# Kernel optimization log

Hardware: AMD Instinct MI355X
Metric: run time of the kernel (lower is better)

The kernel has to match this reference:

```python
import math
import jax, jax.numpy as jnp
import numpy as np

EMBED_DIM = 1024
N_HEADS = 16
HEAD_DIM = EMBED_DIM // N_HEADS
B, T = 4, 2048


def setup_inputs() -> dict:
    key = jax.random.key(0)
    k1, k2, k3 = jax.random.split(key, 3)
    scale_in = 1.0 / math.sqrt(EMBED_DIM)
    return {
        "x": jax.random.normal(k1, (B, T, EMBED_DIM), dtype=jnp.float32),
        "direction": 0,  # 0=FORWARD (causal), 1=RETRODICTION (anti-causal), 2=CORRECTION (causal)
        "qkv_w": jax.random.normal(k2, (EMBED_DIM, 3 * EMBED_DIM), dtype=jnp.float32) * scale_in,
        "qkv_b": jnp.zeros((3 * EMBED_DIM,), dtype=jnp.float32),
        "proj_w": jax.random.normal(k3, (EMBED_DIM, EMBED_DIM), dtype=jnp.float32) * scale_in,
        "proj_b": jnp.zeros((EMBED_DIM,), dtype=jnp.float32),
    }


def reference(x, direction, qkv_w, qkv_b, proj_w, proj_b):
    Bx, Tx, C = x.shape
    qkv = x @ qkv_w + qkv_b                        # [B,T,3C]
    q, k, v = jnp.split(qkv, 3, axis=-1)
    # [B,T,C] -> [B,H,T,D]
    def heads(t):
        return t.reshape(Bx, Tx, N_HEADS, HEAD_DIM).transpose(0, 2, 1, 3)
    q, k, v = heads(q), heads(k), heads(v)
    scale = 1.0 / math.sqrt(HEAD_DIM)
    attn = jnp.einsum('bhqd,bhkd->bhqk', q, k) * scale
    rows = jnp.arange(Tx)[:, None]
    cols = jnp.arange(Tx)[None, :]
    if direction == 1:  # RETRODICTION -> anti-causal (upper triangular allowed)
        mask = cols >= rows
    else:               # FORWARD / CORRECTION -> causal
        mask = cols <= rows
    attn = jnp.where(mask[None, None], attn, -jnp.inf)
    attn = jax.nn.softmax(attn, axis=-1)  # dropout p=0 -> identity
    out = jnp.einsum('bhqk,bhkd->bhqd', attn, v)   # [B,H,T,D]
    out = out.transpose(0, 2, 1, 3).reshape(Bx, Tx, C)
    return out @ proj_w + proj_b
```

## Files before the change

kernel.cpp:

```cpp
#include <hip/hip_runtime.h>
#include <math.h>

typedef __bf16 bf16_t;
typedef bf16_t bf16x8 __attribute__((ext_vector_type(8)));
typedef bf16_t bf16x4 __attribute__((ext_vector_type(4)));
typedef float  f32x4  __attribute__((ext_vector_type(4)));
typedef float  floatv4 __attribute__((ext_vector_type(4)));

#define AS1 __attribute__((address_space(1)))
#define AS3 __attribute__((address_space(3)))

static __device__ __forceinline__ void gld_lds16(const void* g, void* l) {
  __builtin_amdgcn_global_load_lds((const AS1 unsigned int*)g,
                                   (AS3 unsigned int*)l, 16, 0, 0);
}
static __device__ __forceinline__ void block_sync() {
  asm volatile("" ::: "memory");
  __builtin_amdgcn_s_barrier();
  asm volatile("" ::: "memory");
}

__global__ __launch_bounds__(256) void k_cast(const float* __restrict__ in,
                                              bf16_t* __restrict__ out, int n4) {
  int i = blockIdx.x * 256 + threadIdx.x;
  if (i >= n4) return;
  floatv4 v = ((const floatv4*)in)[i];
  bf16x4 o;
  o.x = (bf16_t)v.x; o.y = (bf16_t)v.y; o.z = (bf16_t)v.z; o.w = (bf16_t)v.w;
  ((bf16x4*)out)[i] = o;
}

__global__ __launch_bounds__(256) void k_transpose_cast(const float* __restrict__ in,
                                                        bf16_t* __restrict__ out,
                                                        int R, int Cc) {
  __shared__ float tile[32][33];
  int c0 = blockIdx.x * 32, r0 = blockIdx.y * 32;
  int tx = threadIdx.x, ty = threadIdx.y;
#pragma unroll
  for (int i = 0; i < 32; i += 8)
    tile[ty + i][tx] = in[(size_t)(r0 + ty + i) * Cc + c0 + tx];
  __syncthreads();
#pragma unroll
  for (int i = 0; i < 32; i += 8)
    out[(size_t)(c0 + ty + i) * R + r0 + tx] = (bf16_t)tile[tx][ty + i];
}

__global__ __launch_bounds__(256) void k_gemm_qkv(
    const bf16_t* __restrict__ A, const bf16_t* __restrict__ Bt,
    const float* __restrict__ bias,
    bf16_t* __restrict__ qo, bf16_t* __restrict__ ko, bf16_t* __restrict__ vto) {
  const int K = 1024;
  __shared__ __align__(16) char smem[33792];
  const int m0 = blockIdx.x * 128, n0 = blockIdx.y * 128;
  const int t = threadIdx.x, lane = t & 63, w = t >> 6;
  const int wr = w >> 1, wc = w & 1;
  const int ln15 = lane & 15, lhi = lane >> 4;

  f32x4 acc[4][4];
#pragma unroll
  for (int m = 0; m < 4; ++m)
#pragma unroll
    for (int n = 0; n < 4; ++n) acc[m][n] = (f32x4){0.f, 0.f, 0.f, 0.f};

  const bf16_t* aSrc = A + (size_t)(m0 + w * 16 + ln15) * K + lhi * 8;
  const bf16_t* bSrc = Bt + (size_t)(n0 + w * 16 + ln15) * K + lhi * 8;
  char* dstA = smem + t * 16;

  auto stageG = [&](int k0, int buf) {
    char* base = dstA + buf * 16384;
    gld_lds16(aSrc + k0, base);
    gld_lds16(aSrc + 64 * K + k0, base + 4096);
    gld_lds16(bSrc + k0, base + 8192);
    gld_lds16(bSrc + 64 * K + k0, base + 12288);
  };

  stageG(0, 0);
  asm volatile("s_waitcnt vmcnt(0)" ::: "memory");
  block_sync();
  int buf = 0;
#pragma unroll 2
  for (int it = 0; it < 32; ++it) {
    if (it + 1 < 32) stageG((it + 1) * 32, buf ^ 1);
    const bf16_t* Asb = (const bf16_t*)(smem + buf * 16384);
    const bf16_t* Bsb = (const bf16_t*)(smem + buf * 16384 + 8192);
    bf16x8 af[4], bfr[4];
#pragma unroll
    for (int m = 0; m < 4; ++m)
      af[m] = *(const bf16x8*)(Asb + (wr * 4 + m) * 512 + lane * 8);
#pragma unroll
    for (int n = 0; n < 4; ++n)
      bfr[n] = *(const bf16x8*)(Bsb + (wc * 4 + n) * 512 + lane * 8);
#pragma unroll
    for (int m = 0; m < 4; ++m)
#pragma unroll
      for (int n = 0; n < 4; ++n)
        acc[m][n] = __builtin_amdgcn_mfma_f32_16x16x32_bf16(af[m], bfr[n], acc[m][n], 0, 0, 0);
    asm volatile("s_waitcnt vmcnt(0)" ::: "memory");
    block_sync();
    buf ^= 1;
  }

  bf16_t* L = (bf16_t*)smem;
  const int which = n0 >> 10;
  const float bscale = (which == 0) ? 0.18033688011112042f : 1.0f;
#pragma unroll
  for (int n = 0; n < 4; ++n) {
    const int col = wc * 64 + n * 16 + ln15;
    const float bv = bias[n0 + col];
#pragma unroll
    for (int m = 0; m < 4; ++m)
#pragma unroll
      for (int j = 0; j < 4; ++j) {
        const int row = wr * 64 + m * 16 + lhi * 4 + j;
        const bf16_t ob = (bf16_t)((acc[m][n][j] + bv) * bscale);
        if (which == 2) L[col * 132 + row] = ob;
        else            L[row * 132 + col] = ob;
      }
  }
  block_sync();
  const int bq = m0 >> 11, ttb = m0 & 2047;
  if (which == 2) {
#pragma unroll
    for (int c = 0; c < 8; ++c) {
      const int idx = c * 256 + t;
      const int vcol = idx >> 4, r8 = (idx & 15) * 8;
      bf16x8 v8 = *(const bf16x8*)&L[vcol * 132 + r8];
      const int cc = (n0 + vcol) & 1023;
      const int hh = cc >> 6, d = cc & 63;
      *(bf16x8*)&vto[((size_t)(bq * 16 + hh) * 64 + d) * 2048 + ttb + r8] = v8;
    }
  } else {
    bf16_t* dst = (which == 0) ? qo : ko;
#pragma unroll
    for (int c = 0; c < 8; ++c) {
      const int idx = c * 256 + t;
      const int row = idx >> 4, c8 = (idx & 15) * 8;
      bf16x8 v8 = *(const bf16x8*)&L[row * 132 + c8];
      const int cc = (n0 & 1023) + c8;
      const int hh = cc >> 6, d = cc & 63;
      *(bf16x8*)&dst[((size_t)(bq * 16 + hh) * 2048 + ttb + row) * 64 + d] = v8;
    }
  }
}

__global__ __launch_bounds__(256) void k_attn3(
    const bf16_t* __restrict__ q, const bf16_t* __restrict__ k,
    const bf16_t* __restrict__ vt, const int* __restrict__ dirp,
    bf16_t* __restrict__ a2) {
  const int T = 2048;
  __shared__ __align__(16) bf16_t smem[16384];
  const int bh = blockIdx.x, b = bh >> 4, h = bh & 15;
  const int jb = blockIdx.y;
  const int t = threadIdx.x, lane = t & 63, w = t >> 6;
  const int ln15 = lane & 15, lhi = lane >> 4;
  const bool anti = (*dirp == 1);

  const bf16_t* kbase = k + (size_t)bh * T * 64;
  const bf16_t* vbase = vt + (size_t)bh * 64 * T;

  auto stage = [&](int kc0, int buf) {
    char* Kd = (char*)smem + buf * 16384;
    char* Vd = Kd + 8192;
#pragma unroll
    for (int s = 0; s < 2; ++s) {
      const int qk = s * 4 + (t >> 6);
      const int krow = kc0 + (qk >> 2) * 32 + ((qk >> 1) & 1) * 4 +
                       ((lane & 15) >> 2) * 8 + (lane & 3);
      const int kcolb = (lane >> 4) * 16 + (qk & 1) * 64;
      gld_lds16((const char*)kbase + (size_t)krow * 128 + kcolb,
                Kd + s * 4096 + t * 16);
      const int gv = qk;
      const int vd = (gv & 3) * 16 + (lane & 15);
      gld_lds16((const char*)vbase + (size_t)vd * 4096 + (size_t)kc0 * 2 +
                    (gv >> 2) * 64 + (lane >> 4) * 16,
                Vd + s * 4096 + t * 16);
    }
  };

#pragma unroll 1
  for (int sel = 0; sel < 2; ++sel) {
    const int qt = sel ? (31 - jb) : jb;
    const int q0 = qt * 64 + w * 16;
    const int qrow = q0 + ln15;

    const bf16_t* qp = q + ((size_t)bh * T + qrow) * 64 + lhi * 8;
    bf16x8 qf0 = *(const bf16x8*)qp;
    bf16x8 qf1 = *(const bf16x8*)(qp + 32);

    f32x4 acc[4];
#pragma unroll
    for (int g = 0; g < 4; ++g) acc[g] = (f32x4){0.f, 0.f, 0.f, 0.f};
    float mrun = -3.0e38f, lrun = 0.f;

    const int kt0 = anti ? qt : 0;
    const int nb = anti ? (32 - qt) : (qt + 1);

    stage(kt0 * 64, 0);
#pragma unroll 1
    for (int i = 0; i < nb; ++i) {
      const int kt = kt0 + i;
      const int buf = i & 1;
      if (i + 1 < nb) {
        stage((kt + 1) * 64, buf ^ 1);
        asm volatile("s_waitcnt vmcnt(4)" ::: "memory");
      } else {
        asm volatile("s_waitcnt vmcnt(0)" ::: "memory");
      }
      block_sync();
      const bf16_t* Kb = smem + buf * 8192;
      const bf16_t* Vb = Kb + 4096;

      float sc[16];
#pragma unroll
      for (int kh = 0; kh < 2; ++kh) {
        bf16x8 k0 = *(const bf16x8*)(Kb + (kh * 4 + 0) * 512 + lane * 8);
        bf16x8 k1 = *(const bf16x8*)(Kb + (kh * 4 + 1) * 512 + lane * 8);
        bf16x8 k2 = *(const bf16x8*)(Kb + (kh * 4 + 2) * 512 + lane * 8);
        bf16x8 k3 = *(const bf16x8*)(Kb + (kh * 4 + 3) * 512 + lane * 8);
        const f32x4 zz = (f32x4){0.f, 0.f, 0.f, 0.f};
        f32x4 slo = __builtin_amdgcn_mfma_f32_16x16x32_bf16(k0, qf0, zz, 0, 0, 0);
        slo = __builtin_amdgcn_mfma_f32_16x16x32_bf16(k1, qf1, slo, 0, 0, 0);
        f32x4 shi = __builtin_amdgcn_mfma_f32_16x16x32_bf16(k2, qf0, zz, 0, 0, 0);
        shi = __builtin_amdgcn_mfma_f32_16x16x32_bf16(k3, qf1, shi, 0, 0, 0);
#pragma unroll
        for (int j = 0; j < 4; ++j) {
          sc[kh * 8 + j] = slo[j];
          sc[kh * 8 + 4 + j] = shi[j];
        }
      }
      if (kt == qt) {
#pragma unroll
        for (int e = 0; e < 16; ++e) {
          const int col = kt * 64 + (e >> 3) * 32 + lhi * 8 + (e & 7);
          const bool ok = anti ? (col >= qrow) : (col <= qrow);
          sc[e] = ok ? sc[e] : -3.0e38f;
        }
      }
      float lmax = sc[0];
#pragma unroll
      for (int e = 1; e < 16; ++e) lmax = fmaxf(lmax, sc[e]);
      if (!__all(lmax <= mrun + 8.f)) {
        float vm = lmax;
        vm = fmaxf(vm, __shfl_xor(vm, 16));
        vm = fmaxf(vm, __shfl_xor(vm, 32));
        const float mn = fmaxf(mrun, vm);
        const float al = __builtin_amdgcn_exp2f(mrun - mn);
        lrun *= al;
#pragma unroll
        for (int g = 0; g < 4; ++g) acc[g] *= al;
        mrun = mn;
      }
      bf16x8 pb0, pb1;
      float rs = 0.f;
#pragma unroll
      for (int e = 0; e < 8; ++e) {
        float p = __builtin_amdgcn_exp2f(sc[e] - mrun);
        rs += p; pb0[e] = (bf16_t)p;
      }
#pragma unroll
      for (int e = 0; e < 8; ++e) {
        float p = __builtin_amdgcn_exp2f(sc[8 + e] - mrun);
        rs += p; pb1[e] = (bf16_t)p;
      }
      lrun += rs;
#pragma unroll
      for (int dg = 0; dg < 4; ++dg) {
        bf16x8 v0 = *(const bf16x8*)(Vb + dg * 512 + lane * 8);
        acc[dg] = __builtin_amdgcn_mfma_f32_16x16x32_bf16(v0, pb0, acc[dg], 0, 0, 0);
      }
#pragma unroll
      for (int dg = 0; dg < 4; ++dg) {
        bf16x8 v1 = *(const bf16x8*)(Vb + (4 + dg) * 512 + lane * 8);
        acc[dg] = __builtin_amdgcn_mfma_f32_16x16x32_bf16(v1, pb1, acc[dg], 0, 0, 0);
      }
      block_sync();
    }

    lrun += __shfl_xor(lrun, 16);
    lrun += __shfl_xor(lrun, 32);
    const float inv = __builtin_amdgcn_rcpf(lrun);
    bf16_t* op = a2 + ((size_t)b * T + qrow) * 1024 + h * 64 + lhi * 4;
#pragma unroll
    for (int g = 0; g < 4; ++g) {
      bf16x4 o4;
#pragma unroll
      for (int jx = 0; jx < 4; ++jx) o4[jx] = (bf16_t)(acc[g][jx] * inv);
      *(bf16x4*)(op + g * 16) = o4;
    }
  }
}

__global__ __launch_bounds__(256) void k_gemm_proj(
    const bf16_t* __restrict__ A, const bf16_t* __restrict__ Bt,
    const float* __restrict__ bias, float* __restrict__ out) {
  const int K = 1024;
  __shared__ __align__(16) char smem[32768];
  const int m0 = blockIdx.x * 128, n0 = blockIdx.y * 128;
  const int t = threadIdx.x, lane = t & 63, w = t >> 6;
  const int wr = w >> 1, wc = w & 1;
  const int ln15 = lane & 15, lhi = lane >> 4;

  f32x4 acc[4][4];
#pragma unroll
  for (int m = 0; m < 4; ++m)
#pragma unroll
    for (int n = 0; n < 4; ++n) acc[m][n] = (f32x4){0.f, 0.f, 0.f, 0.f};

  const bf16_t* aSrc = A + (size_t)(m0 + w * 16 + ln15) * K + lhi * 8;
  const bf16_t* bSrc = Bt + (size_t)(n0 + w * 16 + ln15) * K + lhi * 8;
  char* dstA = smem + t * 16;

  auto stageG = [&](int k0, int buf) {
    char* base = dstA + buf * 16384;
    gld_lds16(aSrc + k0, base);
    gld_lds16(aSrc + 64 * K + k0, base + 4096);
    gld_lds16(bSrc + k0, base + 8192);
    gld_lds16(bSrc + 64 * K + k0, base + 12288);
  };

  stageG(0, 0);
  asm volatile("s_waitcnt vmcnt(0)" ::: "memory");
  block_sync();
  int buf = 0;
#pragma unroll 2
  for (int it = 0; it < 32; ++it) {
    if (it + 1 < 32) stageG((it + 1) * 32, buf ^ 1);
    const bf16_t* Asb = (const bf16_t*)(smem + buf * 16384);
    const bf16_t* Bsb = (const bf16_t*)(smem + buf * 16384 + 8192);
    bf16x8 af[4], bfr[4];
#pragma unroll
    for (int m = 0; m < 4; ++m)
      af[m] = *(const bf16x8*)(Asb + (wr * 4 + m) * 512 + lane * 8);
#pragma unroll
    for (int n = 0; n < 4; ++n)
      bfr[n] = *(const bf16x8*)(Bsb + (wc * 4 + n) * 512 + lane * 8);
#pragma unroll
    for (int m = 0; m < 4; ++m)
#pragma unroll
      for (int n = 0; n < 4; ++n)
        acc[m][n] = __builtin_amdgcn_mfma_f32_16x16x32_bf16(af[m], bfr[n], acc[m][n], 0, 0, 0);
    asm volatile("s_waitcnt vmcnt(0)" ::: "memory");
    block_sync();
    buf ^= 1;
  }
#pragma unroll
  for (int n = 0; n < 4; ++n) {
    const int col = n0 + wc * 64 + n * 16 + ln15;
    const float bv = bias[col];
#pragma unroll
    for (int m = 0; m < 4; ++m)
#pragma unroll
      for (int j = 0; j < 4; ++j) {
        const int row = m0 + wr * 64 + m * 16 + lhi * 4 + j;
        out[(size_t)row * 1024 + col] = acc[m][n][j] + bv;
      }
  }
}

extern "C" void kernel_launch(void* const* d_in, const int* in_sizes, int n_in,
                              void* d_out, int out_size, void* d_ws, size_t ws_size,
                              hipStream_t stream) {
  (void)in_sizes; (void)n_in; (void)out_size; (void)ws_size;
  const float* x      = (const float*)d_in[0];
  const int*   dirp   = (const int*)d_in[1];
  const float* qkv_w  = (const float*)d_in[2];
  const float* qkv_b  = (const float*)d_in[3];
  const float* proj_w = (const float*)d_in[4];
  const float* proj_b = (const float*)d_in[5];
  float* out = (float*)d_out;

  char* ws = (char*)d_ws;
  bf16_t* xb   = (bf16_t*)(ws);
  bf16_t* wq_t = (bf16_t*)(ws + 16777216);
  bf16_t* wp_t = (bf16_t*)(ws + 23068672);
  bf16_t* qb   = (bf16_t*)(ws + 25165824);
  bf16_t* kb   = (bf16_t*)(ws + 41943040);
  bf16_t* vtb  = (bf16_t*)(ws + 58720256);
  bf16_t* a2   = xb;

  k_cast<<<8192, 256, 0, stream>>>(x, xb, 2097152);
  k_transpose_cast<<<dim3(96, 32), dim3(32, 8), 0, stream>>>(qkv_w, wq_t, 1024, 3072);
  k_transpose_cast<<<dim3(32, 32), dim3(32, 8), 0, stream>>>(proj_w, wp_t, 1024, 1024);
  k_gemm_qkv<<<dim3(64, 24), 256, 0, stream>>>(xb, wq_t, qkv_b, qb, kb, vtb);
  k_attn3<<<dim3(64, 16), 256, 0, stream>>>(qb, kb, vtb, dirp, a2);
  k_gemm_proj<<<dim3(64, 8), 256, 0, stream>>>(a2, wp_t, proj_b, out);
}
```

Measured before the change: 223.5 us.

## Enlarge GEMM tiles to 256x128 with 512 threads and triple-buffered BK=64 pipeline

Both the QKV and output-projection GEMMs move from 128x128 tiles with 256 threads, BK=32 and double buffering to 256x128 tiles with 512 threads (8 waves), BK=64 and a three-stage global-to-LDS pipeline. Partial vmcnt waits let two stages of loads stay in flight while one is computed, and s_setprio raises wave priority around the MFMA bursts. The aim is more reuse per LDS load, fewer barriers per unit of K, and better hiding of global latency. The cost is about 144KB of LDS per block, which allows only one block per CU. The projection grid shrinks to 256 blocks, which lowers occupancy and may leave load imbalance.

```diff
diff --git a/kernel.cpp b/kernel.cpp
--- a/kernel.cpp
+++ b/kernel.cpp
@@ -45,16 +45,17 @@
     out[(size_t)(c0 + ty + i) * R + r0 + tx] = (bf16_t)tile[tx][ty + i];
 }
 
-__global__ __launch_bounds__(256) void k_gemm_qkv(
+
+__global__ __launch_bounds__(512, 2) void k_gemm_qkv(
     const bf16_t* __restrict__ A, const bf16_t* __restrict__ Bt,
     const float* __restrict__ bias,
     bf16_t* __restrict__ qo, bf16_t* __restrict__ ko, bf16_t* __restrict__ vto) {
   const int K = 1024;
-  __shared__ __align__(16) char smem[33792];
-  const int m0 = blockIdx.x * 128, n0 = blockIdx.y * 128;
-  const int t = threadIdx.x, lane = t & 63, w = t >> 6;
-  const int wr = w >> 1, wc = w & 1;
+  __shared__ __align__(16) char smem[147456];
+  const int m0 = blockIdx.x * 256, n0 = blockIdx.y * 128;
+  const int t = threadIdx.x, lane = t & 63, wv = t >> 6;
   const int ln15 = lane & 15, lhi = lane >> 4;
+  const int wr = wv >> 1, wc = wv & 1;
 
   f32x4 acc[4][4];
 #pragma unroll
@@ -62,47 +63,64 @@
 #pragma unroll
     for (int n = 0; n < 4; ++n) acc[m][n] = (f32x4){0.f, 0.f, 0.f, 0.f};
 
-  const bf16_t* aSrc = A + (size_t)(m0 + w * 16 + ln15) * K + lhi * 8;
-  const bf16_t* bSrc = Bt + (size_t)(n0 + w * 16 + ln15) * K + lhi * 8;
-  char* dstA = smem + t * 16;
-
-  auto stageG = [&](int k0, int buf) {
-    char* base = dstA + buf * 16384;
-    gld_lds16(aSrc + k0, base);
-    gld_lds16(aSrc + 64 * K + k0, base + 4096);
-    gld_lds16(bSrc + k0, base + 8192);
-    gld_lds16(bSrc + 64 * K + k0, base + 12288);
+  const bf16_t* aSrc = A + (size_t)(m0 + (t >> 7) * 16 + ln15) * K + ((t >> 6) & 1) * 32 + lhi * 8;
+  const bf16_t* bSrc = Bt + (size_t)(n0 + (t >> 7) * 16 + ln15) * K + ((t >> 6) & 1) * 32 + lhi * 8;
+  const int dstOff = t * 16;
+
+  auto stage = [&](int k0, char* base) {
+#pragma unroll
+    for (int c = 0; c < 4; ++c)
+      gld_lds16(aSrc + (size_t)c * 64 * K + k0, base + c * 8192 + dstOff);
+#pragma unroll
+    for (int c = 0; c < 2; ++c)
+      gld_lds16(bSrc + (size_t)c * 64 * K + k0, base + 32768 + c * 8192 + dstOff);
   };
-
-  stageG(0, 0);
-  asm volatile("s_waitcnt vmcnt(0)" ::: "memory");
-  block_sync();
-  int buf = 0;
-#pragma unroll 2
-  for (int it = 0; it < 32; ++it) {
-    if (it + 1 < 32) stageG((it + 1) * 32, buf ^ 1);
-    const bf16_t* Asb = (const bf16_t*)(smem + buf * 16384);
-    const bf16_t* Bsb = (const bf16_t*)(smem + buf * 16384 + 8192);
-    bf16x8 af[4], bfr[4];
-#pragma unroll
-    for (int m = 0; m < 4; ++m)
-      af[m] = *(const bf16x8*)(Asb + (wr * 4 + m) * 512 + lane * 8);
-#pragma unroll
-    for (int n = 0; n < 4; ++n)
-      bfr[n] = *(const bf16x8*)(Bsb + (wc * 4 + n) * 512 + lane * 8);
-#pragma unroll
-    for (int m = 0; m < 4; ++m)
+  auto compute = [&](const char* base) {
+    const bf16_t* Ab = (const bf16_t*)base;
+    const bf16_t* Bb = (const bf16_t*)(base + 32768);
+#pragma unroll
+    for (int kk = 0; kk < 2; ++kk) {
+      bf16x8 af[4], bf[4];
+#pragma unroll
+      for (int m = 0; m < 4; ++m)
+        af[m] = *(const bf16x8*)(Ab + ((wr * 4 + m) * 2 + kk) * 512 + lane * 8);
 #pragma unroll
       for (int n = 0; n < 4; ++n)
-        acc[m][n] = __builtin_amdgcn_mfma_f32_16x16x32_bf16(af[m], bfr[n], acc[m][n], 0, 0, 0);
-    asm volatile("s_waitcnt vmcnt(0)" ::: "memory");
+        bf[n] = *(const bf16x8*)(Bb + ((wc * 4 + n) * 2 + kk) * 512 + lane * 8);
+      __builtin_amdgcn_s_setprio(1);
+#pragma unroll
+      for (int m = 0; m < 4; ++m)
+#pragma unroll
+        for (int n = 0; n < 4; ++n)
+          acc[m][n] = __builtin_amdgcn_mfma_f32_16x16x32_bf16(af[m], bf[n], acc[m][n], 0, 0, 0);
+      __builtin_amdgcn_s_setprio(0);
+    }
+  };
+
+  char* pc = smem;
+  char* p1 = smem + 49152;
+  char* p2 = smem + 98304;
+  stage(0, pc);
+  stage(64, p1);
+#pragma unroll 1
+  for (int it = 0; it < 16; ++it) {
+    if (it + 2 < 16) {
+      stage((it + 2) * 64, p2);
+      asm volatile("s_waitcnt vmcnt(12)" ::: "memory");
+    } else if (it + 1 < 16) {
+      asm volatile("s_waitcnt vmcnt(6)" ::: "memory");
+    } else {
+      asm volatile("s_waitcnt vmcnt(0)" ::: "memory");
+    }
     block_sync();
-    buf ^= 1;
-  }
-
-  bf16_t* L = (bf16_t*)smem;
+    compute(pc);
+    block_sync();
+    char* old = pc; pc = p1; p1 = p2; p2 = old;
+  }
+
   const int which = n0 >> 10;
   const float bscale = (which == 0) ? 0.18033688011112042f : 1.0f;
+  bf16_t* L = (bf16_t*)smem;
 #pragma unroll
   for (int n = 0; n < 4; ++n) {
     const int col = wc * 64 + n * 16 + ln15;
@@ -113,7 +131,7 @@
       for (int j = 0; j < 4; ++j) {
         const int row = wr * 64 + m * 16 + lhi * 4 + j;
         const bf16_t ob = (bf16_t)((acc[m][n][j] + bv) * bscale);
-        if (which == 2) L[col * 132 + row] = ob;
+        if (which == 2) L[col * 264 + row] = ob;
         else            L[row * 132 + col] = ob;
       }
   }
@@ -122,9 +140,9 @@
   if (which == 2) {
 #pragma unroll
     for (int c = 0; c < 8; ++c) {
-      const int idx = c * 256 + t;
-      const int vcol = idx >> 4, r8 = (idx & 15) * 8;
-      bf16x8 v8 = *(const bf16x8*)&L[vcol * 132 + r8];
+      const int idx = c * 512 + t;
+      const int vcol = idx >> 5, r8 = (idx & 31) * 8;
+      bf16x8 v8 = *(const bf16x8*)&L[vcol * 264 + r8];
       const int cc = (n0 + vcol) & 1023;
       const int hh = cc >> 6, d = cc & 63;
       *(bf16x8*)&vto[((size_t)(bq * 16 + hh) * 64 + d) * 2048 + ttb + r8] = v8;
@@ -133,7 +151,7 @@
     bf16_t* dst = (which == 0) ? qo : ko;
 #pragma unroll
     for (int c = 0; c < 8; ++c) {
-      const int idx = c * 256 + t;
+      const int idx = c * 512 + t;
       const int row = idx >> 4, c8 = (idx & 15) * 8;
       bf16x8 v8 = *(const bf16x8*)&L[row * 132 + c8];
       const int cc = (n0 & 1023) + c8;
@@ -290,15 +308,15 @@
   }
 }
 
-__global__ __launch_bounds__(256) void k_gemm_proj(
+__global__ __launch_bounds__(512, 2) void k_gemm_proj(
     const bf16_t* __restrict__ A, const bf16_t* __restrict__ Bt,
     const float* __restrict__ bias, float* __restrict__ out) {
   const int K = 1024;
-  __shared__ __align__(16) char smem[32768];
-  const int m0 = blockIdx.x * 128, n0 = blockIdx.y * 128;
-  const int t = threadIdx.x, lane = t & 63, w = t >> 6;
-  const int wr = w >> 1, wc = w & 1;
+  __shared__ __align__(16) char smem[147456];
+  const int m0 = blockIdx.x * 256, n0 = blockIdx.y * 128;
+  const int t = threadIdx.x, lane = t & 63, wv = t >> 6;
   const int ln15 = lane & 15, lhi = lane >> 4;
+  const int wr = wv >> 1, wc = wv & 1;
 
   f32x4 acc[4][4];
 #pragma unroll
@@ -306,43 +324,61 @@
 #pragma unroll
     for (int n = 0; n < 4; ++n) acc[m][n] = (f32x4){0.f, 0.f, 0.f, 0.f};
 
-  const bf16_t* aSrc = A + (size_t)(m0 + w * 16 + ln15) * K + lhi * 8;
-  const bf16_t* bSrc = Bt + (size_t)(n0 + w * 16 + ln15) * K + lhi * 8;
-  char* dstA = smem + t * 16;
-
-  auto stageG = [&](int k0, int buf) {
-    char* base = dstA + buf * 16384;
-    gld_lds16(aSrc + k0, base);
-    gld_lds16(aSrc + 64 * K + k0, base + 4096);
-    gld_lds16(bSrc + k0, base + 8192);
-    gld_lds16(bSrc + 64 * K + k0, base + 12288);
+  const bf16_t* aSrc = A + (size_t)(m0 + (t >> 7) * 16 + ln15) * K + ((t >> 6) & 1) * 32 + lhi * 8;
+  const bf16_t* bSrc = Bt + (size_t)(n0 + (t >> 7) * 16 + ln15) * K + ((t >> 6) & 1) * 32 + lhi * 8;
+  const int dstOff = t * 16;
+
+  auto stage = [&](int k0, char* base) {
+#pragma unroll
+    for (int c = 0; c < 4; ++c)
+      gld_lds16(aSrc + (size_t)c * 64 * K + k0, base + c * 8192 + dstOff);
+#pragma unroll
+    for (int c = 0; c < 2; ++c)
+      gld_lds16(bSrc + (size_t)c * 64 * K + k0, base + 32768 + c * 8192 + dstOff);
   };
-
-  stageG(0, 0);
-  asm volatile("s_waitcnt vmcnt(0)" ::: "memory");
-  block_sync();
-  int buf = 0;
-#pragma unroll 2
-  for (int it = 0; it < 32; ++it) {
-    if (it + 1 < 32) stageG((it + 1) * 32, buf ^ 1);
-    const bf16_t* Asb = (const bf16_t*)(smem + buf * 16384);
-    const bf16_t* Bsb = (const bf16_t*)(smem + buf * 16384 + 8192);
-    bf16x8 af[4], bfr[4];
-#pragma unroll
-    for (int m = 0; m < 4; ++m)
-      af[m] = *(const bf16x8*)(Asb + (wr * 4 + m) * 512 + lane * 8);
-#pragma unroll
-    for (int n = 0; n < 4; ++n)
-      bfr[n] = *(const bf16x8*)(Bsb + (wc * 4 + n) * 512 + lane * 8);
-#pragma unroll
-    for (int m = 0; m < 4; ++m)
+  auto compute = [&](const char* base) {
+    const bf16_t* Ab = (const bf16_t*)base;
+    const bf16_t* Bb = (const bf16_t*)(base + 32768);
+#pragma unroll
+    for (int kk = 0; kk < 2; ++kk) {
+      bf16x8 af[4], bf[4];
+#pragma unroll
+      for (int m = 0; m < 4; ++m)
+        af[m] = *(const bf16x8*)(Ab + ((wr * 4 + m) * 2 + kk) * 512 + lane * 8);
 #pragma unroll
       for (int n = 0; n < 4; ++n)
-        acc[m][n] = __builtin_amdgcn_mfma_f32_16x16x32_bf16(af[m], bfr[n], acc[m][n], 0, 0, 0);
-    asm volatile("s_waitcnt vmcnt(0)" ::: "memory");
+        bf[n] = *(const bf16x8*)(Bb + ((wc * 4 + n) * 2 + kk) * 512 + lane * 8);
+      __builtin_amdgcn_s_setprio(1);
+#pragma unroll
+      for (int m = 0; m < 4; ++m)
+#pragma unroll
+        for (int n = 0; n < 4; ++n)
+          acc[m][n] = __builtin_amdgcn_mfma_f32_16x16x32_bf16(af[m], bf[n], acc[m][n], 0, 0, 0);
+      __builtin_amdgcn_s_setprio(0);
+    }
+  };
+
+  char* pc = smem;
+  char* p1 = smem + 49152;
+  char* p2 = smem + 98304;
+  stage(0, pc);
+  stage(64, p1);
+#pragma unroll 1
+  for (int it = 0; it < 16; ++it) {
+    if (it + 2 < 16) {
+      stage((it + 2) * 64, p2);
+      asm volatile("s_waitcnt vmcnt(12)" ::: "memory");
+    } else if (it + 1 < 16) {
+      asm volatile("s_waitcnt vmcnt(6)" ::: "memory");
+    } else {
+      asm volatile("s_waitcnt vmcnt(0)" ::: "memory");
+    }
     block_sync();
-    buf ^= 1;
-  }
+    compute(pc);
+    block_sync();
+    char* old = pc; pc = p1; p1 = p2; p2 = old;
+  }
+
 #pragma unroll
   for (int n = 0; n < 4; ++n) {
     const int col = n0 + wc * 64 + n * 16 + ln15;
@@ -381,7 +417,7 @@
   k_cast<<<8192, 256, 0, stream>>>(x, xb, 2097152);
   k_transpose_cast<<<dim3(96, 32), dim3(32, 8), 0, stream>>>(qkv_w, wq_t, 1024, 3072);
   k_transpose_cast<<<dim3(32, 32), dim3(32, 8), 0, stream>>>(proj_w, wp_t, 1024, 1024);
-  k_gemm_qkv<<<dim3(64, 24), 256, 0, stream>>>(xb, wq_t, qkv_b, qb, kb, vtb);
+  k_gemm_qkv<<<dim3(32, 24), 512, 0, stream>>>(xb, wq_t, qkv_b, qb, kb, vtb);
   k_attn3<<<dim3(64, 16), 256, 0, stream>>>(qb, kb, vtb, dirp, a2);
-  k_gemm_proj<<<dim3(64, 8), 256, 0, stream>>>(a2, wp_t, proj_b, out);
-}
+  k_gemm_proj<<<dim3(32, 8), 512, 0, stream>>>(a2, wp_t, proj_b, out);
+}
```

Result: faster. 204.5 us (-8.5%).

## Widen QKV GEMM tile to 128x256 and add MFMA priority scheduling

Applied to the files above, without the earlier changes.

The QKV projection GEMM now computes a 128x256 output tile per block, with each wave owning a 128x64 strip so the A fragments are shared across a wider N. This halves the grid and raises reuse of each A load. Both GEMMs also wait on LDS explicitly, raise wave priority around the MFMA bursts, and set launch_bounds occupancy to 3. The epilogue is now split into two passes through LDS. Risks are higher register pressure from 32 accumulators per wave, fewer blocks in flight, and extra barriers in the epilogue.

```diff
diff --git a/kernel.cpp b/kernel.cpp
--- a/kernel.cpp
+++ b/kernel.cpp
@@ -45,101 +45,116 @@
     out[(size_t)(c0 + ty + i) * R + r0 + tx] = (bf16_t)tile[tx][ty + i];
 }
 
-__global__ __launch_bounds__(256) void k_gemm_qkv(
+
+__global__ __launch_bounds__(256, 3) void k_gemm_qkv(
     const bf16_t* __restrict__ A, const bf16_t* __restrict__ Bt,
     const float* __restrict__ bias,
     bf16_t* __restrict__ qo, bf16_t* __restrict__ ko, bf16_t* __restrict__ vto) {
   const int K = 1024;
-  __shared__ __align__(16) char smem[33792];
-  const int m0 = blockIdx.x * 128, n0 = blockIdx.y * 128;
-  const int t = threadIdx.x, lane = t & 63, w = t >> 6;
-  const int wr = w >> 1, wc = w & 1;
+  __shared__ __align__(16) char smem[49152];
+  const int m0 = blockIdx.x * 128, n0 = blockIdx.y * 256;
+  const int t = threadIdx.x, lane = t & 63, wv = t >> 6;
   const int ln15 = lane & 15, lhi = lane >> 4;
 
-  f32x4 acc[4][4];
-#pragma unroll
-  for (int m = 0; m < 4; ++m)
+  f32x4 acc[8][4];
+#pragma unroll
+  for (int m = 0; m < 8; ++m)
 #pragma unroll
     for (int n = 0; n < 4; ++n) acc[m][n] = (f32x4){0.f, 0.f, 0.f, 0.f};
 
-  const bf16_t* aSrc = A + (size_t)(m0 + w * 16 + ln15) * K + lhi * 8;
-  const bf16_t* bSrc = Bt + (size_t)(n0 + w * 16 + ln15) * K + lhi * 8;
-  char* dstA = smem + t * 16;
-
-  auto stageG = [&](int k0, int buf) {
-    char* base = dstA + buf * 16384;
-    gld_lds16(aSrc + k0, base);
-    gld_lds16(aSrc + 64 * K + k0, base + 4096);
-    gld_lds16(bSrc + k0, base + 8192);
-    gld_lds16(bSrc + 64 * K + k0, base + 12288);
+  const bf16_t* aS = A + (size_t)(m0 + wv * 16 + ln15) * K + lhi * 8;
+  const bf16_t* bS = Bt + (size_t)(n0 + wv * 16 + ln15) * K + lhi * 8;
+
+  auto stage = [&](int k0, char* buf) {
+    gld_lds16(aS + k0, buf + t * 16);
+    gld_lds16(aS + (size_t)64 * K + k0, buf + 4096 + t * 16);
+#pragma unroll
+    for (int r = 0; r < 4; ++r)
+      gld_lds16(bS + (size_t)r * 64 * K + k0, buf + 8192 + r * 4096 + t * 16);
   };
 
-  stageG(0, 0);
+  stage(0, smem);
   asm volatile("s_waitcnt vmcnt(0)" ::: "memory");
   block_sync();
-  int buf = 0;
-#pragma unroll 2
+
+#pragma unroll 1
   for (int it = 0; it < 32; ++it) {
-    if (it + 1 < 32) stageG((it + 1) * 32, buf ^ 1);
-    const bf16_t* Asb = (const bf16_t*)(smem + buf * 16384);
-    const bf16_t* Bsb = (const bf16_t*)(smem + buf * 16384 + 8192);
+    char* bufC = smem + (it & 1) * 24576;
+    char* bufN = smem + ((it + 1) & 1) * 24576;
+    if (it + 1 < 32) stage((it + 1) * 32, bufN);
+    const bf16_t* Ab = (const bf16_t*)bufC;
+    const bf16_t* Bb = (const bf16_t*)(bufC + 8192);
     bf16x8 af[4], bfr[4];
 #pragma unroll
-    for (int m = 0; m < 4; ++m)
-      af[m] = *(const bf16x8*)(Asb + (wr * 4 + m) * 512 + lane * 8);
-#pragma unroll
     for (int n = 0; n < 4; ++n)
-      bfr[n] = *(const bf16x8*)(Bsb + (wc * 4 + n) * 512 + lane * 8);
-#pragma unroll
-    for (int m = 0; m < 4; ++m)
-#pragma unroll
-      for (int n = 0; n < 4; ++n)
-        acc[m][n] = __builtin_amdgcn_mfma_f32_16x16x32_bf16(af[m], bfr[n], acc[m][n], 0, 0, 0);
+      bfr[n] = *(const bf16x8*)(Bb + (wv * 4 + n) * 512 + lane * 8);
+#pragma unroll
+    for (int h = 0; h < 2; ++h) {
+#pragma unroll
+      for (int m = 0; m < 4; ++m)
+        af[m] = *(const bf16x8*)(Ab + (h * 4 + m) * 512 + lane * 8);
+      asm volatile("s_waitcnt lgkmcnt(0)" ::: "memory");
+      __builtin_amdgcn_sched_barrier(0);
+      __builtin_amdgcn_s_setprio(1);
+#pragma unroll
+      for (int m = 0; m < 4; ++m)
+#pragma unroll
+        for (int n = 0; n < 4; ++n)
+          acc[h * 4 + m][n] = __builtin_amdgcn_mfma_f32_16x16x32_bf16(af[m], bfr[n], acc[h * 4 + m][n], 0, 0, 0);
+      __builtin_amdgcn_s_setprio(0);
+    }
     asm volatile("s_waitcnt vmcnt(0)" ::: "memory");
     block_sync();
-    buf ^= 1;
   }
 
   bf16_t* L = (bf16_t*)smem;
-  const int which = n0 >> 10;
-  const float bscale = (which == 0) ? 0.18033688011112042f : 1.0f;
-#pragma unroll
-  for (int n = 0; n < 4; ++n) {
-    const int col = wc * 64 + n * 16 + ln15;
-    const float bv = bias[n0 + col];
-#pragma unroll
-    for (int m = 0; m < 4; ++m)
-#pragma unroll
-      for (int j = 0; j < 4; ++j) {
-        const int row = wr * 64 + m * 16 + lhi * 4 + j;
-        const bf16_t ob = (bf16_t)((acc[m][n][j] + bv) * bscale);
-        if (which == 2) L[col * 132 + row] = ob;
-        else            L[row * 132 + col] = ob;
-      }
-  }
-  block_sync();
   const int bq = m0 >> 11, ttb = m0 & 2047;
-  if (which == 2) {
-#pragma unroll
-    for (int c = 0; c < 8; ++c) {
-      const int idx = c * 256 + t;
-      const int vcol = idx >> 4, r8 = (idx & 15) * 8;
-      bf16x8 v8 = *(const bf16x8*)&L[vcol * 132 + r8];
-      const int cc = (n0 + vcol) & 1023;
-      const int hh = cc >> 6, d = cc & 63;
-      *(bf16x8*)&vto[((size_t)(bq * 16 + hh) * 64 + d) * 2048 + ttb + r8] = v8;
-    }
-  } else {
-    bf16_t* dst = (which == 0) ? qo : ko;
-#pragma unroll
-    for (int c = 0; c < 8; ++c) {
-      const int idx = c * 256 + t;
-      const int row = idx >> 4, c8 = (idx & 15) * 8;
-      bf16x8 v8 = *(const bf16x8*)&L[row * 132 + c8];
-      const int cc = (n0 & 1023) + c8;
-      const int hh = cc >> 6, d = cc & 63;
-      *(bf16x8*)&dst[((size_t)(bq * 16 + hh) * 2048 + ttb + row) * 64 + d] = v8;
-    }
+  const int whichw = (n0 + (wv & 1) * 64 + (wv >> 1) * 128) >> 10;
+  (void)whichw;
+#pragma unroll 1
+  for (int p = 0; p < 2; ++p) {
+    const int whichp = (n0 + p * 128) >> 10;
+    const float bscale = (whichp == 0) ? 0.18033688011112042f : 1.0f;
+    if ((wv >> 1) == p) {
+#pragma unroll
+      for (int n = 0; n < 4; ++n) {
+        const int colL = (wv & 1) * 64 + n * 16 + ln15;
+        const float bv = bias[n0 + p * 128 + colL];
+#pragma unroll
+        for (int m = 0; m < 8; ++m)
+#pragma unroll
+          for (int j = 0; j < 4; ++j) {
+            const int row = m * 16 + lhi * 4 + j;
+            const bf16_t ob = (bf16_t)((acc[m][n][j] + bv) * bscale);
+            if (whichp == 2) L[colL * 132 + row] = ob;
+            else             L[row * 132 + colL] = ob;
+          }
+      }
+    }
+    block_sync();
+    if (whichp == 2) {
+#pragma unroll
+      for (int c = 0; c < 8; ++c) {
+        const int idx = c * 256 + t;
+        const int vcol = idx >> 4, r8 = (idx & 15) * 8;
+        bf16x8 v8 = *(const bf16x8*)&L[vcol * 132 + r8];
+        const int cc = (n0 + p * 128 + vcol) & 1023;
+        const int hh = cc >> 6, d = cc & 63;
+        *(bf16x8*)&vto[((size_t)(bq * 16 + hh) * 64 + d) * 2048 + ttb + r8] = v8;
+      }
+    } else {
+      bf16_t* dst = (whichp == 0) ? qo : ko;
+#pragma unroll
+      for (int c = 0; c < 8; ++c) {
+        const int idx = c * 256 + t;
+        const int row = idx >> 4, c8 = (idx & 15) * 8;
+        bf16x8 v8 = *(const bf16x8*)&L[row * 132 + c8];
+        const int cc = ((n0 & 1023) + p * 128) + c8;
+        const int hh = cc >> 6, d = cc & 63;
+        *(bf16x8*)&dst[((size_t)(bq * 16 + hh) * 2048 + ttb + row) * 64 + d] = v8;
+      }
+    }
+    block_sync();
   }
 }
 
@@ -290,15 +305,15 @@
   }
 }
 
-__global__ __launch_bounds__(256) void k_gemm_proj(
+__global__ __launch_bounds__(256, 3) void k_gemm_proj(
     const bf16_t* __restrict__ A, const bf16_t* __restrict__ Bt,
     const float* __restrict__ bias, float* __restrict__ out) {
   const int K = 1024;
   __shared__ __align__(16) char smem[32768];
   const int m0 = blockIdx.x * 128, n0 = blockIdx.y * 128;
-  const int t = threadIdx.x, lane = t & 63, w = t >> 6;
-  const int wr = w >> 1, wc = w & 1;
+  const int t = threadIdx.x, lane = t & 63, wv = t >> 6;
   const int ln15 = lane & 15, lhi = lane >> 4;
+  const int wr = wv >> 1, wcn = wv & 1;
 
   f32x4 acc[4][4];
 #pragma unroll
@@ -306,46 +321,50 @@
 #pragma unroll
     for (int n = 0; n < 4; ++n) acc[m][n] = (f32x4){0.f, 0.f, 0.f, 0.f};
 
-  const bf16_t* aSrc = A + (size_t)(m0 + w * 16 + ln15) * K + lhi * 8;
-  const bf16_t* bSrc = Bt + (size_t)(n0 + w * 16 + ln15) * K + lhi * 8;
-  char* dstA = smem + t * 16;
-
-  auto stageG = [&](int k0, int buf) {
-    char* base = dstA + buf * 16384;
-    gld_lds16(aSrc + k0, base);
-    gld_lds16(aSrc + 64 * K + k0, base + 4096);
-    gld_lds16(bSrc + k0, base + 8192);
-    gld_lds16(bSrc + 64 * K + k0, base + 12288);
+  const bf16_t* aS = A + (size_t)(m0 + wv * 16 + ln15) * K + lhi * 8;
+  const bf16_t* bS = Bt + (size_t)(n0 + wv * 16 + ln15) * K + lhi * 8;
+
+  auto stage = [&](int k0, char* buf) {
+    gld_lds16(aS + k0, buf + t * 16);
+    gld_lds16(aS + (size_t)64 * K + k0, buf + 4096 + t * 16);
+    gld_lds16(bS + k0, buf + 8192 + t * 16);
+    gld_lds16(bS + (size_t)64 * K + k0, buf + 12288 + t * 16);
   };
 
-  stageG(0, 0);
+  stage(0, smem);
   asm volatile("s_waitcnt vmcnt(0)" ::: "memory");
   block_sync();
-  int buf = 0;
-#pragma unroll 2
+
+#pragma unroll 1
   for (int it = 0; it < 32; ++it) {
-    if (it + 1 < 32) stageG((it + 1) * 32, buf ^ 1);
-    const bf16_t* Asb = (const bf16_t*)(smem + buf * 16384);
-    const bf16_t* Bsb = (const bf16_t*)(smem + buf * 16384 + 8192);
+    char* bufC = smem + (it & 1) * 16384;
+    char* bufN = smem + ((it + 1) & 1) * 16384;
+    if (it + 1 < 32) stage((it + 1) * 32, bufN);
+    const bf16_t* Ab = (const bf16_t*)bufC;
+    const bf16_t* Bb = (const bf16_t*)(bufC + 8192);
     bf16x8 af[4], bfr[4];
 #pragma unroll
     for (int m = 0; m < 4; ++m)
-      af[m] = *(const bf16x8*)(Asb + (wr * 4 + m) * 512 + lane * 8);
+      af[m] = *(const bf16x8*)(Ab + (wr * 4 + m) * 512 + lane * 8);
 #pragma unroll
     for (int n = 0; n < 4; ++n)
-      bfr[n] = *(const bf16x8*)(Bsb + (wc * 4 + n) * 512 + lane * 8);
+      bfr[n] = *(const bf16x8*)(Bb + (wcn * 4 + n) * 512 + lane * 8);
+    asm volatile("s_waitcnt lgkmcnt(0)" ::: "memory");
+    __builtin_amdgcn_sched_barrier(0);
+    __builtin_amdgcn_s_setprio(1);
 #pragma unroll
     for (int m = 0; m < 4; ++m)
 #pragma unroll
       for (int n = 0; n < 4; ++n)
         acc[m][n] = __builtin_amdgcn_mfma_f32_16x16x32_bf16(af[m], bfr[n], acc[m][n], 0, 0, 0);
+    __builtin_amdgcn_s_setprio(0);
     asm volatile("s_waitcnt vmcnt(0)" ::: "memory");
     block_sync();
-    buf ^= 1;
   }
+
 #pragma unroll
   for (int n = 0; n < 4; ++n) {
-    const int col = n0 + wc * 64 + n * 16 + ln15;
+    const int col = n0 + wcn * 64 + n * 16 + ln15;
     const float bv = bias[col];
 #pragma unroll
     for (int m = 0; m < 4; ++m)
@@ -381,7 +400,7 @@
   k_cast<<<8192, 256, 0, stream>>>(x, xb, 2097152);
   k_transpose_cast<<<dim3(96, 32), dim3(32, 8), 0, stream>>>(qkv_w, wq_t, 1024, 3072);
   k_transpose_cast<<<dim3(32, 32), dim3(32, 8), 0, stream>>>(proj_w, wp_t, 1024, 1024);
-  k_gemm_qkv<<<dim3(64, 24), 256, 0, stream>>>(xb, wq_t, qkv_b, qb, kb, vtb);
+  k_gemm_qkv<<<dim3(64, 12), 256, 0, stream>>>(xb, wq_t, qkv_b, qb, kb, vtb);
   k_attn3<<<dim3(64, 16), 256, 0, stream>>>(qb, kb, vtb, dirp, a2);
   k_gemm_proj<<<dim3(64, 8), 256, 0, stream>>>(a2, wp_t, proj_b, out);
 }
```

Result: slower. 230.0 us (+2.9%).
